# Optimization experiments

Measured on AMD Instinct MI355X. Metric: run time of the kernel, lower is better.

Reference implementation:

```python
import jax, jax.numpy as jnp
import numpy as np

B, NS, S, H = 512, 2, 128, 768
DS, NL = 384, 40
TEMP, ALPHA, GAMMA = 0.05, 0.15, 7.5
EPS = 1e-8


def setup_inputs() -> dict:
    key = jax.random.key(0)
    ks = jax.random.split(key, 8)
    return {
        "bert_emb": jax.random.normal(ks[0], (B, NS, S, H), dtype=jnp.float32),
        "rel_desc_emb": jax.random.normal(ks[1], (B, DS), dtype=jnp.float32),
        "dense_w": 0.02 * jax.random.normal(ks[2], (H, H), dtype=jnp.float32),
        "dense_b": jnp.zeros((H,), dtype=jnp.float32),
        "cls_w": 0.02 * jax.random.normal(ks[3], (3 * H, NL), dtype=jnp.float32),
        "cls_b": jnp.zeros((NL,), dtype=jnp.float32),
        "fc_w": 0.02 * jax.random.normal(ks[4], (3 * H, DS), dtype=jnp.float32),
        "fc_b": jnp.zeros((DS,), dtype=jnp.float32),
        "entity_idx": jax.random.randint(ks[5], (B, NS, 2), 0, S, dtype=jnp.int64 if jax.config.jax_enable_x64 else jnp.int32),
        "classify_labels": jax.random.randint(ks[6], (B,), 0, NL, dtype=jnp.int64 if jax.config.jax_enable_x64 else jnp.int32),
    }


def _mean_ce(logits, labels):
    lp = jax.nn.log_softmax(logits, axis=-1)
    return -jnp.mean(jnp.take_along_axis(lp, labels[:, None], axis=1))


def _l2n(x):
    return x / jnp.maximum(jnp.linalg.norm(x, axis=-1, keepdims=True), EPS)


def reference(bert_emb, rel_desc_emb, dense_w, dense_b, cls_w, cls_b, fc_w, fc_b,
              entity_idx, classify_labels):
    b = bert_emb.shape[0]
    bidx = jnp.arange(b)
    # ----- relation representation from sentence 0 (cls | head | tail) -----
    s0 = bert_emb[:, 0]                                   # [B,S,H]
    cls_tok = s0[:, 0]                                    # [B,H]
    head = s0[bidx, entity_idx[:, 0, 0]]                  # [B,H]
    tail = s0[bidx, entity_idx[:, 0, 1]]                  # [B,H]
    relation_hidden = jnp.tanh(jnp.concatenate([cls_tok, head, tail], axis=-1))  # [B,3H]
    logits = relation_hidden @ cls_w + cls_b              # [B,NL]
    ce_loss = _mean_ce(logits, classify_labels)
    # ----- margin loss vs relation-description embeddings (cosine) -----
    rel_emb = relation_hidden @ fc_w + fc_b               # [B,DS]
    C = _l2n(rel_emb) @ _l2n(rel_desc_emb).T              # [B,B] cosine sims
    pos = jnp.diagonal(C)
    diff_label = classify_labels[:, None] != classify_labels[None, :]
    neg = jnp.max(jnp.where(diff_label, C, -jnp.inf), axis=1)
    neg = jnp.maximum(neg, 0.0)                           # max_val initialized at 0
    margin_loss = jnp.sum(jax.nn.relu(neg - pos + GAMMA)) * (1.0 - ALPHA)
    ce_loss = ce_loss + margin_loss
    # ----- contrastive loss on (head|tail) entity pairs from both sents -----
    # dense is token-wise; apply only to the 4 gathered tokens per example
    h1a = bert_emb[bidx, 0, entity_idx[:, 0, 0]]
    h1b = bert_emb[bidx, 0, entity_idx[:, 0, 1]]
    h2a = bert_emb[bidx, 1, entity_idx[:, 1, 0]]
    h2b = bert_emb[bidx, 1, entity_idx[:, 1, 1]]
    toks = jnp.stack([h1a, h1b, h2a, h2b], axis=1)        # [B,4,H]
    toks = jnp.tanh(toks @ dense_w + dense_b)             # [B,4,H]
    z1 = toks[:, 0:2].reshape(b, -1)                      # [B,2H]
    z2 = toks[:, 2:4].reshape(b, -1)                      # [B,2H]
    cos_sim = (_l2n(z1) @ _l2n(z2).T) / TEMP              # [B,B]
    cl_loss = _mean_ce(cos_sim, bidx)
    return ce_loss + ALPHA * cl_loss
```

## Files before the change

### kernel.cpp

```cpp
#include <hip/hip_runtime.h>
#include <hip/hip_bf16.h>
#include <math.h>

#define B_   512
#define NS_  2
#define S_   128
#define H_   768
#define DS_  384
#define NL_  40
#define H3_  (3*H_)
#define TEMP_ 0.05f
#define ALPHA_ 0.15f
#define GAMMA_ 7.5f
#define EPS_ 1e-8f

typedef __attribute__((ext_vector_type(8))) short bf8_t;
typedef __attribute__((ext_vector_type(4))) float f4_t;

#define LDSPAD 40


__device__ __forceinline__ float block_reduce_sum(float v, float* sh) {
    int t = threadIdx.x;
    sh[t] = v; __syncthreads();
    for (int s = blockDim.x / 2; s > 0; s >>= 1) {
        if (t < s) sh[t] += sh[t + s];
        __syncthreads();
    }
    float r = sh[0]; __syncthreads();
    return r;
}

__device__ __forceinline__ float block_reduce_max(float v, float* sh) {
    int t = threadIdx.x;
    sh[t] = v; __syncthreads();
    for (int s = blockDim.x / 2; s > 0; s >>= 1) {
        if (t < s) sh[t] = fmaxf(sh[t], sh[t + s]);
        __syncthreads();
    }
    float r = sh[0]; __syncthreads();
    return r;
}

__device__ __forceinline__ void transpose_tile(
    const float* __restrict__ in, __hip_bfloat16* __restrict__ out,
    int K, int N, int kt, int nt, int tid, float* tileLds )
{
    int k0 = kt * 32, n0 = nt * 32;
    int tx = tid & 31, ty = tid >> 5;
#pragma unroll
    for (int i = 0; i < 4; ++i) {
        int k = k0 + ty + i * 8, n = n0 + tx;
        if (k < K && n < N) tileLds[(ty + i*8) * 33 + tx] = in[(size_t)k * N + n];
    }
    __syncthreads();
#pragma unroll
    for (int i = 0; i < 4; ++i) {
        int n = n0 + ty + i * 8, k = k0 + tx;
        if (n < N && k < K) out[(size_t)n * K + k] = __float2bfloat16(tileLds[tx * 33 + ty + i*8]);
    }
}

__global__ __launch_bounds__(256) void prep_kernel(
    const float* __restrict__ bert, const int* __restrict__ eidx,
    const float* __restrict__ dense_w, const float* __restrict__ fc_w,
    const float* __restrict__ cls_w, const float* __restrict__ desc,
    __hip_bfloat16* __restrict__ rh_bf, __hip_bfloat16* __restrict__ toks_bf,
    __hip_bfloat16* __restrict__ dwt, __hip_bfloat16* __restrict__ fwt,
    __hip_bfloat16* __restrict__ cwt, __hip_bfloat16* __restrict__ desc_nb,
    float* __restrict__ acc, int* __restrict__ done)
{
    __shared__ float tileLds[32 * 33];
    int blk = blockIdx.x;
    int t = threadIdx.x;
    if (blk < 512) {
        int b = blk;
        if (b == 0) {
            if (t < 4) acc[t] = 0.0f;
            if (t == 4) *done = 0;
        }
        int e00 = eidx[b*4 + 0];
        int e01 = eidx[b*4 + 1];
        int e10 = eidx[b*4 + 2];
        int e11 = eidx[b*4 + 3];
        const float* s0 = bert + (size_t)b * NS_ * S_ * H_;
        const float* s1 = s0 + (size_t)S_ * H_;
        const float* cls  = s0;
        const float* head = s0 + (size_t)e00 * H_;
        const float* tail = s0 + (size_t)e01 * H_;
        const float* h2a  = s1 + (size_t)e10 * H_;
        const float* h2b  = s1 + (size_t)e11 * H_;
        __hip_bfloat16* rhb = rh_bf + (size_t)b * H3_;
        __hip_bfloat16* tk  = toks_bf + (size_t)b * 4 * H_;
        for (int h = t; h < H_; h += 256) {
            float c  = cls[h];
            float hd = head[h];
            float tl = tail[h];
            rhb[h]        = __float2bfloat16(tanhf(c));
            rhb[H_ + h]   = __float2bfloat16(tanhf(hd));
            rhb[2*H_ + h] = __float2bfloat16(tanhf(tl));
            tk[h]         = __float2bfloat16(hd);
            tk[H_ + h]    = __float2bfloat16(tl);
            tk[2*H_ + h]  = __float2bfloat16(h2a[h]);
            tk[3*H_ + h]  = __float2bfloat16(h2b[h]);
        }
    } else if (blk < 1088) {
        int q = blk - 512;
        transpose_tile(dense_w, dwt, H_, H_, q / 24, q % 24, t, tileLds);
    } else if (blk < 1952) {
        int q = blk - 1088;
        transpose_tile(fc_w, fwt, H3_, DS_, q / 12, q % 12, t, tileLds);
    } else if (blk < 2096) {
        int q = blk - 1952;
        int kt = q / 2, nt = q % 2;
        transpose_tile(cls_w, cwt, H3_, NL_, kt, nt, t, tileLds);
        if (nt == 1) {
            int tx = t & 31, ty = t >> 5;
            cwt[(size_t)(40 + ty) * H3_ + kt * 32 + tx] = __float2bfloat16(0.0f);
        }
    } else {
        int i = blk - 2096;
        const float* x = desc + (size_t)i * DS_;
        float ss = 0.0f;
        for (int d = t; d < DS_; d += 256) { float v = x[d]; ss += v * v; }
        ss = block_reduce_sum(ss, tileLds);
        float inv = 1.0f / fmaxf(sqrtf(ss), EPS_);
        __hip_bfloat16* o = desc_nb + (size_t)i * DS_;
        for (int d = t; d < DS_; d += 256) o[d] = __float2bfloat16(x[d] * inv);
    }
}


__device__ __forceinline__ void gemm128_body(
    const __hip_bfloat16* __restrict__ A, const __hip_bfloat16* __restrict__ Bp,
    const float* __restrict__ bias, float* __restrict__ C,
    int K, int lda, int ldb, int ldc, int fuse_tanh, int bx, int by,
    __hip_bfloat16* As, __hip_bfloat16* Bs)
{
    int tid  = threadIdx.x;
    int lane = tid & 63;
    int wave = tid >> 6;
    int wm = (wave >> 1) * 64;
    int wn = (wave & 1) * 64;
    int lr = lane & 15;
    int quad = lane >> 4;
    int rowBase = by * 128;
    int colBase = bx * 128;

    f4_t acc[4][4];
#pragma unroll
    for (int i = 0; i < 4; ++i)
#pragma unroll
        for (int j = 0; j < 4; ++j) acc[i][j] = (f4_t){0.f, 0.f, 0.f, 0.f};

    int sr = tid >> 2, sc = tid & 3;
    for (int k0 = 0; k0 < K; k0 += 32) {
#pragma unroll
        for (int half = 0; half < 2; ++half) {
            int r = sr + half * 64;
            *(bf8_t*)&As[r * LDSPAD + sc * 8] =
                *(const bf8_t*)(A + (size_t)(rowBase + r) * lda + k0 + sc * 8);
            *(bf8_t*)&Bs[r * LDSPAD + sc * 8] =
                *(const bf8_t*)(Bp + (size_t)(colBase + r) * ldb + k0 + sc * 8);
        }
        __syncthreads();
        bf8_t af[4], bfr[4];
#pragma unroll
        for (int f = 0; f < 4; ++f) {
            af[f]  = *(const bf8_t*)&As[(wm + f*16 + lr) * LDSPAD + quad * 8];
            bfr[f] = *(const bf8_t*)&Bs[(wn + f*16 + lr) * LDSPAD + quad * 8];
        }
#pragma unroll
        for (int i = 0; i < 4; ++i)
#pragma unroll
            for (int j = 0; j < 4; ++j)
                acc[i][j] = __builtin_amdgcn_mfma_f32_16x16x32_bf16(af[i], bfr[j], acc[i][j], 0, 0, 0);
        __syncthreads();
    }
#pragma unroll
    for (int j = 0; j < 4; ++j) {
        int col = colBase + wn + j*16 + lr;
        float bv = bias ? bias[col] : 0.0f;
#pragma unroll
        for (int i = 0; i < 4; ++i) {
            int row0 = rowBase + wm + i*16 + quad*4;
#pragma unroll
            for (int r = 0; r < 4; ++r) {
                float v = acc[i][j][r] + bv;
                if (fuse_tanh) v = tanhf(v);
                C[(size_t)(row0 + r) * ldc + col] = v;
            }
        }
    }
}

__device__ __forceinline__ void gemm64_body(
    const __hip_bfloat16* __restrict__ A, const __hip_bfloat16* __restrict__ Bp,
    const float* __restrict__ bias, float* __restrict__ C,
    int K, int lda, int ldb, int ldc, float scale, int bx, int by,
    __hip_bfloat16* As, __hip_bfloat16* Bs)
{
    int tid  = threadIdx.x;
    int lane = tid & 63;
    int wave = tid >> 6;
    int lr = lane & 15;
    int quad = lane >> 4;
    int rowBase = by * 64;
    int colBase = bx * 64;

    f4_t acc[4];
#pragma unroll
    for (int i = 0; i < 4; ++i) acc[i] = (f4_t){0.f, 0.f, 0.f, 0.f};

    int sr = tid >> 2, sc = tid & 3;
    for (int k0 = 0; k0 < K; k0 += 32) {
        *(bf8_t*)&As[sr * LDSPAD + sc * 8] =
            *(const bf8_t*)(A + (size_t)(rowBase + sr) * lda + k0 + sc * 8);
        *(bf8_t*)&Bs[sr * LDSPAD + sc * 8] =
            *(const bf8_t*)(Bp + (size_t)(colBase + sr) * ldb + k0 + sc * 8);
        __syncthreads();
        bf8_t bfr = *(const bf8_t*)&Bs[(wave*16 + lr) * LDSPAD + quad * 8];
#pragma unroll
        for (int f = 0; f < 4; ++f) {
            bf8_t af = *(const bf8_t*)&As[(f*16 + lr) * LDSPAD + quad * 8];
            acc[f] = __builtin_amdgcn_mfma_f32_16x16x32_bf16(af, bfr, acc[f], 0, 0, 0);
        }
        __syncthreads();
    }
    int col = colBase + wave*16 + lr;
    float bv = bias ? bias[col] : 0.0f;
#pragma unroll
    for (int f = 0; f < 4; ++f) {
        int row0 = rowBase + f*16 + quad*4;
#pragma unroll
        for (int r = 0; r < 4; ++r)
            C[(size_t)(row0 + r) * ldc + col] = acc[f][r] * scale + bv;
    }
}

__device__ __forceinline__ void cls_ce_body(
    const __hip_bfloat16* __restrict__ rh, const __hip_bfloat16* __restrict__ cwt,
    const float* __restrict__ cls_b, const int* __restrict__ labels,
    float* __restrict__ acc, int rowBase, float* lgp )
{
    int tid  = threadIdx.x;
    int lane = tid & 63;
    int wave = tid >> 6;
    int lr = lane & 15;
    int quad = lane >> 4;

    f4_t a3[3];
#pragma unroll
    for (int j = 0; j < 3; ++j) a3[j] = (f4_t){0.f, 0.f, 0.f, 0.f};

    int kw0 = wave * (H3_ / 4);
    const __hip_bfloat16* aRow = rh + (size_t)(rowBase + lr) * H3_ + quad * 8;
#pragma unroll 2
    for (int s = 0; s < 18; ++s) {
        int k = kw0 + s * 32;
        bf8_t af = *(const bf8_t*)(aRow + k);
#pragma unroll
        for (int j = 0; j < 3; ++j) {
            bf8_t bfr = *(const bf8_t*)(cwt + (size_t)(j*16 + lr) * H3_ + k + quad * 8);
            a3[j] = __builtin_amdgcn_mfma_f32_16x16x32_bf16(af, bfr, a3[j], 0, 0, 0);
        }
    }
#pragma unroll
    for (int j = 0; j < 3; ++j) {
        int col = j*16 + lr;
#pragma unroll
        for (int r = 0; r < 4; ++r)
            lgp[wave * 768 + (quad*4 + r) * 48 + col] = a3[j][r];
    }
    __syncthreads();
    for (int idx = tid; idx < 768; idx += 256) {
        int col = idx % 48;
        float s = lgp[idx] + lgp[768 + idx] + lgp[1536 + idx] + lgp[2304 + idx];
        s = (col < NL_) ? (s + cls_b[col]) : -INFINITY;
        lgp[idx] = s;
    }
    __syncthreads();
    if (tid < 64) {
        float ce = 0.0f;
        if (tid < 16) {
            const float* Lr = &lgp[tid * 48];
            float m = -INFINITY;
            for (int c = 0; c < NL_; ++c) m = fmaxf(m, Lr[c]);
            float s = 0.0f;
            for (int c = 0; c < NL_; ++c) s += expf(Lr[c] - m);
            ce = logf(s) + m - Lr[labels[rowBase + tid]];
        }
        for (int off = 8; off >= 1; off >>= 1) ce += __shfl_down(ce, off);
        if (tid == 0) atomicAdd(acc + 0, ce * (1.0f / (float)B_));
    }
}

__global__ __launch_bounds__(256) void gemms_kernel(
    const __hip_bfloat16* __restrict__ toks_bf, const __hip_bfloat16* __restrict__ dwt,
    const float* __restrict__ dense_b, float* __restrict__ toks_out,
    const __hip_bfloat16* __restrict__ rh_bf, const __hip_bfloat16* __restrict__ fwt,
    const float* __restrict__ fc_b, float* __restrict__ rel_emb,
    const __hip_bfloat16* __restrict__ cwt, const float* __restrict__ cls_b,
    const int* __restrict__ labels, float* __restrict__ acc)
{
    __shared__ __align__(16) char smem[2 * 128 * LDSPAD * 2];
    int blk = blockIdx.x;
    if (blk < 96) {
        gemm128_body(toks_bf, dwt, dense_b, toks_out, H_, H_, H_, H_, 1,
                     blk % 6, blk / 6,
                     (__hip_bfloat16*)smem, (__hip_bfloat16*)(smem + 128 * LDSPAD * 2));
    } else if (blk < 144) {
        int q = blk - 96;
        gemm64_body(rh_bf, fwt, fc_b, rel_emb, H3_, H3_, H3_, DS_, 1.0f,
                    q % 6, q / 6,
                    (__hip_bfloat16*)smem, (__hip_bfloat16*)(smem + 64 * LDSPAD * 2));
    } else {
        cls_ce_body(rh_bf, cwt, cls_b, labels, acc, (blk - 144) * 16, (float*)smem);
    }
}

__global__ __launch_bounds__(256) void znorm_kernel(
    const float* __restrict__ rel_emb, const float* __restrict__ toks_out,
    __hip_bfloat16* __restrict__ rel_nb, __hip_bfloat16* __restrict__ z_bf)
{
    __shared__ float sh[256];
    int blk = blockIdx.x, t = threadIdx.x;
    const float* x; __hip_bfloat16* o; int D;
    if (blk < 512) { x = rel_emb + (size_t)blk * DS_;          o = rel_nb + (size_t)blk * DS_;        D = DS_; }
    else           { x = toks_out + (size_t)(blk-512) * 2*H_;  o = z_bf + (size_t)(blk-512) * 2*H_;   D = 2*H_; }
    float ss = 0.0f;
    for (int d = t; d < D; d += 256) { float v = x[d]; ss += v * v; }
    ss = block_reduce_sum(ss, sh);
    float inv = 1.0f / fmaxf(sqrtf(ss), EPS_);
    for (int d = t; d < D; d += 256) o[d] = __float2bfloat16(x[d] * inv);
}

__global__ __launch_bounds__(256) void c1c2_kernel(
    const __hip_bfloat16* __restrict__ rel_nb, const __hip_bfloat16* __restrict__ desc_nb,
    const __hip_bfloat16* __restrict__ z_bf, float* __restrict__ C1, float* __restrict__ C2)
{
    __shared__ __align__(16) char smem[2 * 64 * LDSPAD * 2];
    __hip_bfloat16* As = (__hip_bfloat16*)smem;
    __hip_bfloat16* Bs = (__hip_bfloat16*)(smem + 64 * LDSPAD * 2);
    int blk = blockIdx.x;
    if (blk < 64) {
        gemm64_body(rel_nb, desc_nb, (const float*)nullptr, C1, DS_, DS_, DS_, B_, 1.0f,
                    blk % 8, blk / 8, As, Bs);
    } else {
        int q = blk - 64;
        gemm64_body(z_bf, z_bf + 2*H_, (const float*)nullptr, C2, 2*H_, 4*H_, 4*H_, B_, 1.0f/TEMP_,
                    q % 8, q / 8, As, Bs);
    }
}

__global__ __launch_bounds__(256) void tail_kernel(
    const float* __restrict__ C1, const float* __restrict__ C2,
    const int* __restrict__ labels, float* __restrict__ acc,
    int* __restrict__ done, float* __restrict__ out)
{
    __shared__ float sh[256];
    int blk = blockIdx.x, t = threadIdx.x;
    if (blk < 512) {
        int i = blk;
        int li = labels[i];
        const float* row = C1 + (size_t)i * B_;
        float m = -INFINITY;
        for (int j = t; j < B_; j += 256)
            if (labels[j] != li) m = fmaxf(m, row[j]);
        float negmax = block_reduce_max(m, sh);
        if (t == 0) {
            float neg = fmaxf(negmax, 0.0f);
            float term = neg - row[i] + GAMMA_;
            if (term > 0.0f) atomicAdd(acc + 1, term);
        }
    } else {
        int i = blk - 512;
        const float* row = C2 + (size_t)i * B_;
        float m = -INFINITY;
        for (int j = t; j < B_; j += 256) m = fmaxf(m, row[j]);
        m = block_reduce_max(m, sh);
        float s = 0.0f;
        for (int j = t; j < B_; j += 256) s += expf(row[j] - m);
        s = block_reduce_sum(s, sh);
        if (t == 0) atomicAdd(acc + 2, (logf(s) + m - row[i]) * (1.0f / (float)B_));
    }
    __threadfence();
    if (t == 0) {
        int prev = atomicAdd(done, 1);
        if (prev == 1023) {
            float a0 = atomicAdd(acc + 0, 0.0f);
            float a1 = atomicAdd(acc + 1, 0.0f);
            float a2 = atomicAdd(acc + 2, 0.0f);
            out[0] = a0 + (1.0f - ALPHA_) * a1 + ALPHA_ * a2;
        }
    }
}


extern "C" void kernel_launch(void* const* d_in, const int* in_sizes, int n_in,
                              void* d_out, int out_size, void* d_ws, size_t ws_size,
                              hipStream_t stream) {
    const float* bert     = (const float*)d_in[0];
    const float* desc     = (const float*)d_in[1];
    const float* dense_w  = (const float*)d_in[2];
    const float* dense_b  = (const float*)d_in[3];
    const float* cls_w    = (const float*)d_in[4];
    const float* cls_b    = (const float*)d_in[5];
    const float* fc_w     = (const float*)d_in[6];
    const float* fc_b     = (const float*)d_in[7];
    const int*   eidx     = (const int*)d_in[8];
    const int*   labels   = (const int*)d_in[9];
    float* out = (float*)d_out;

    float* fp = (float*)d_ws;
    __hip_bfloat16* rh_bf   = (__hip_bfloat16*)fp; fp += (size_t)B_*H3_/2;
    __hip_bfloat16* toks_bf = (__hip_bfloat16*)fp; fp += (size_t)B_*4*H_/2;
    __hip_bfloat16* dwt_bf  = (__hip_bfloat16*)fp; fp += (size_t)H_*H_/2;
    __hip_bfloat16* fwt_bf  = (__hip_bfloat16*)fp; fp += (size_t)DS_*H3_/2;
    __hip_bfloat16* cwt_bf  = (__hip_bfloat16*)fp; fp += (size_t)48*H3_/2;
    __hip_bfloat16* desc_nb = (__hip_bfloat16*)fp; fp += (size_t)B_*DS_/2;
    __hip_bfloat16* rel_nb  = (__hip_bfloat16*)fp; fp += (size_t)B_*DS_/2;
    __hip_bfloat16* z_bf    = (__hip_bfloat16*)fp; fp += (size_t)B_*4*H_/2;
    float* toks_out = fp; fp += (size_t)B_*4*H_;
    float* rel_emb  = fp; fp += (size_t)B_*DS_;
    float* C1       = fp; fp += (size_t)B_*B_;
    float* C2       = fp; fp += (size_t)B_*B_;
    float* acc      = fp; fp += 4;
    int*   done     = (int*)fp;

    prep_kernel<<<2608, 256, 0, stream>>>(bert, eidx, dense_w, fc_w, cls_w, desc,
                                          rh_bf, toks_bf, dwt_bf, fwt_bf, cwt_bf,
                                          desc_nb, acc, done);

    gemms_kernel<<<176, 256, 0, stream>>>(toks_bf, dwt_bf, dense_b, toks_out,
                                          rh_bf, fwt_bf, fc_b, rel_emb,
                                          cwt_bf, cls_b, labels, acc);

    znorm_kernel<<<1536, 256, 0, stream>>>(rel_emb, toks_out, rel_nb, z_bf);

    c1c2_kernel<<<128, 256, 0, stream>>>(rel_nb, desc_nb, z_bf, C1, C2);

    tail_kernel<<<1024, 256, 0, stream>>>(C1, C2, labels, acc, done, out);
}
```

Baseline: 571.7 us.

## Double-buffer GEMM LDS tiles, split-K small GEMMs, shuffle-based reductions

Both GEMM bodies now use double-buffered LDS and prefetch the next K tile into registers while MFMAs run, so there is one barrier per iteration instead of two. The fc GEMM and the z GEMM are split along K into two halves written to separate partial buffers, which gives the grid more blocks. The halves are summed, with the bias added, in znorm and tail. Block reductions switch to wave shuffles plus a 4-entry LDS combine, and znorm and tail use vectorized loads with fixed per-thread element counts. This costs extra workspace and extra partial-buffer traffic, and it doubles LDS per block.

```diff
diff --git a/kernel.cpp b/kernel.cpp
--- a/kernel.cpp
+++ b/kernel.cpp
@@ -15,30 +15,36 @@
 #define EPS_ 1e-8f
 
 typedef __attribute__((ext_vector_type(8))) short bf8_t;
+typedef __attribute__((ext_vector_type(4))) short s4_t;
 typedef __attribute__((ext_vector_type(4))) float f4_t;
 
 #define LDSPAD 40
 
 
+__device__ __forceinline__ short bfbits(float x) {
+    __hip_bfloat16 h = __float2bfloat16(x);
+    return *reinterpret_cast<short*>(&h);
+}
+
 __device__ __forceinline__ float block_reduce_sum(float v, float* sh) {
-    int t = threadIdx.x;
-    sh[t] = v; __syncthreads();
-    for (int s = blockDim.x / 2; s > 0; s >>= 1) {
-        if (t < s) sh[t] += sh[t + s];
-        __syncthreads();
-    }
-    float r = sh[0]; __syncthreads();
+#pragma unroll
+    for (int off = 32; off >= 1; off >>= 1) v += __shfl_down(v, off, 64);
+    int w = threadIdx.x >> 6;
+    if ((threadIdx.x & 63) == 0) sh[w] = v;
+    __syncthreads();
+    float r = (sh[0] + sh[1]) + (sh[2] + sh[3]);
+    __syncthreads();
     return r;
 }
 
 __device__ __forceinline__ float block_reduce_max(float v, float* sh) {
-    int t = threadIdx.x;
-    sh[t] = v; __syncthreads();
-    for (int s = blockDim.x / 2; s > 0; s >>= 1) {
-        if (t < s) sh[t] = fmaxf(sh[t], sh[t + s]);
-        __syncthreads();
-    }
-    float r = sh[0]; __syncthreads();
+#pragma unroll
+    for (int off = 32; off >= 1; off >>= 1) v = fmaxf(v, __shfl_down(v, off, 64));
+    int w = threadIdx.x >> 6;
+    if ((threadIdx.x & 63) == 0) sh[w] = v;
+    __syncthreads();
+    float r = fmaxf(fmaxf(sh[0], sh[1]), fmaxf(sh[2], sh[3]));
+    __syncthreads();
     return r;
 }
 
@@ -135,7 +141,8 @@
     const __hip_bfloat16* __restrict__ A, const __hip_bfloat16* __restrict__ Bp,
     const float* __restrict__ bias, float* __restrict__ C,
     int K, int lda, int ldb, int ldc, int fuse_tanh, int bx, int by,
-    __hip_bfloat16* As, __hip_bfloat16* Bs)
+    __hip_bfloat16* As0, __hip_bfloat16* Bs0,
+    __hip_bfloat16* As1, __hip_bfloat16* Bs1)
 {
     int tid  = threadIdx.x;
     int lane = tid & 63;
@@ -154,27 +161,48 @@
         for (int j = 0; j < 4; ++j) acc[i][j] = (f4_t){0.f, 0.f, 0.f, 0.f};
 
     int sr = tid >> 2, sc = tid & 3;
-    for (int k0 = 0; k0 < K; k0 += 32) {
-#pragma unroll
-        for (int half = 0; half < 2; ++half) {
-            int r = sr + half * 64;
-            *(bf8_t*)&As[r * LDSPAD + sc * 8] =
-                *(const bf8_t*)(A + (size_t)(rowBase + r) * lda + k0 + sc * 8);
-            *(bf8_t*)&Bs[r * LDSPAD + sc * 8] =
-                *(const bf8_t*)(Bp + (size_t)(colBase + r) * ldb + k0 + sc * 8);
-        }
-        __syncthreads();
+    const __hip_bfloat16* Abase = A + (size_t)(rowBase + sr) * lda + sc * 8;
+    const __hip_bfloat16* Bbase = Bp + (size_t)(colBase + sr) * ldb + sc * 8;
+    size_t a64 = (size_t)64 * lda, b64 = (size_t)64 * ldb;
+
+    *(bf8_t*)&As0[sr * LDSPAD + sc * 8]        = *(const bf8_t*)(Abase);
+    *(bf8_t*)&As0[(sr + 64) * LDSPAD + sc * 8] = *(const bf8_t*)(Abase + a64);
+    *(bf8_t*)&Bs0[sr * LDSPAD + sc * 8]        = *(const bf8_t*)(Bbase);
+    *(bf8_t*)&Bs0[(sr + 64) * LDSPAD + sc * 8] = *(const bf8_t*)(Bbase + b64);
+    __syncthreads();
+
+    int nIter = K >> 5;
+    for (int i = 0; i < nIter; ++i) {
+        __hip_bfloat16* Asc = (i & 1) ? As1 : As0;
+        __hip_bfloat16* Bsc = (i & 1) ? Bs1 : Bs0;
+        __hip_bfloat16* Asn = (i & 1) ? As0 : As1;
+        __hip_bfloat16* Bsn = (i & 1) ? Bs0 : Bs1;
+        bf8_t pa0, pa1, pb0, pb1;
+        bool pf = (i + 1 < nIter);
+        if (pf) {
+            int k = (i + 1) << 5;
+            pa0 = *(const bf8_t*)(Abase + k);
+            pa1 = *(const bf8_t*)(Abase + a64 + k);
+            pb0 = *(const bf8_t*)(Bbase + k);
+            pb1 = *(const bf8_t*)(Bbase + b64 + k);
+        }
         bf8_t af[4], bfr[4];
 #pragma unroll
         for (int f = 0; f < 4; ++f) {
-            af[f]  = *(const bf8_t*)&As[(wm + f*16 + lr) * LDSPAD + quad * 8];
-            bfr[f] = *(const bf8_t*)&Bs[(wn + f*16 + lr) * LDSPAD + quad * 8];
-        }
-#pragma unroll
-        for (int i = 0; i < 4; ++i)
+            af[f]  = *(const bf8_t*)&Asc[(wm + f*16 + lr) * LDSPAD + quad * 8];
+            bfr[f] = *(const bf8_t*)&Bsc[(wn + f*16 + lr) * LDSPAD + quad * 8];
+        }
+#pragma unroll
+        for (int ii = 0; ii < 4; ++ii)
 #pragma unroll
             for (int j = 0; j < 4; ++j)
-                acc[i][j] = __builtin_amdgcn_mfma_f32_16x16x32_bf16(af[i], bfr[j], acc[i][j], 0, 0, 0);
+                acc[ii][j] = __builtin_amdgcn_mfma_f32_16x16x32_bf16(af[ii], bfr[j], acc[ii][j], 0, 0, 0);
+        if (pf) {
+            *(bf8_t*)&Asn[sr * LDSPAD + sc * 8]        = pa0;
+            *(bf8_t*)&Asn[(sr + 64) * LDSPAD + sc * 8] = pa1;
+            *(bf8_t*)&Bsn[sr * LDSPAD + sc * 8]        = pb0;
+            *(bf8_t*)&Bsn[(sr + 64) * LDSPAD + sc * 8] = pb1;
+        }
         __syncthreads();
     }
 #pragma unroll
@@ -196,9 +224,10 @@
 
 __device__ __forceinline__ void gemm64_body(
     const __hip_bfloat16* __restrict__ A, const __hip_bfloat16* __restrict__ Bp,
-    const float* __restrict__ bias, float* __restrict__ C,
-    int K, int lda, int ldb, int ldc, float scale, int bx, int by,
-    __hip_bfloat16* As, __hip_bfloat16* Bs)
+    float* __restrict__ C,
+    int K, int kBase, int lda, int ldb, int ldc, float scale, int bx, int by,
+    __hip_bfloat16* As0, __hip_bfloat16* Bs0,
+    __hip_bfloat16* As1, __hip_bfloat16* Bs1)
 {
     int tid  = threadIdx.x;
     int lane = tid & 63;
@@ -213,28 +242,45 @@
     for (int i = 0; i < 4; ++i) acc[i] = (f4_t){0.f, 0.f, 0.f, 0.f};
 
     int sr = tid >> 2, sc = tid & 3;
-    for (int k0 = 0; k0 < K; k0 += 32) {
-        *(bf8_t*)&As[sr * LDSPAD + sc * 8] =
-            *(const bf8_t*)(A + (size_t)(rowBase + sr) * lda + k0 + sc * 8);
-        *(bf8_t*)&Bs[sr * LDSPAD + sc * 8] =
-            *(const bf8_t*)(Bp + (size_t)(colBase + sr) * ldb + k0 + sc * 8);
+    const __hip_bfloat16* Abase = A + (size_t)(rowBase + sr) * lda + kBase + sc * 8;
+    const __hip_bfloat16* Bbase = Bp + (size_t)(colBase + sr) * ldb + kBase + sc * 8;
+
+    *(bf8_t*)&As0[sr * LDSPAD + sc * 8] = *(const bf8_t*)(Abase);
+    *(bf8_t*)&Bs0[sr * LDSPAD + sc * 8] = *(const bf8_t*)(Bbase);
+    __syncthreads();
+
+    int nIter = K >> 5;
+    for (int i = 0; i < nIter; ++i) {
+        __hip_bfloat16* Asc = (i & 1) ? As1 : As0;
+        __hip_bfloat16* Bsc = (i & 1) ? Bs1 : Bs0;
+        __hip_bfloat16* Asn = (i & 1) ? As0 : As1;
+        __hip_bfloat16* Bsn = (i & 1) ? Bs0 : Bs1;
+        bf8_t pa, pb;
+        bool pf = (i + 1 < nIter);
+        if (pf) {
+            int k = (i + 1) << 5;
+            pa = *(const bf8_t*)(Abase + k);
+            pb = *(const bf8_t*)(Bbase + k);
+        }
+        bf8_t bfr = *(const bf8_t*)&Bsc[(wave*16 + lr) * LDSPAD + quad * 8];
+#pragma unroll
+        for (int f = 0; f < 4; ++f) {
+            bf8_t af = *(const bf8_t*)&Asc[(f*16 + lr) * LDSPAD + quad * 8];
+            acc[f] = __builtin_amdgcn_mfma_f32_16x16x32_bf16(af, bfr, acc[f], 0, 0, 0);
+        }
+        if (pf) {
+            *(bf8_t*)&Asn[sr * LDSPAD + sc * 8] = pa;
+            *(bf8_t*)&Bsn[sr * LDSPAD + sc * 8] = pb;
+        }
         __syncthreads();
-        bf8_t bfr = *(const bf8_t*)&Bs[(wave*16 + lr) * LDSPAD + quad * 8];
-#pragma unroll
-        for (int f = 0; f < 4; ++f) {
-            bf8_t af = *(const bf8_t*)&As[(f*16 + lr) * LDSPAD + quad * 8];
-            acc[f] = __builtin_amdgcn_mfma_f32_16x16x32_bf16(af, bfr, acc[f], 0, 0, 0);
-        }
-        __syncthreads();
     }
     int col = colBase + wave*16 + lr;
-    float bv = bias ? bias[col] : 0.0f;
 #pragma unroll
     for (int f = 0; f < 4; ++f) {
         int row0 = rowBase + f*16 + quad*4;
 #pragma unroll
         for (int r = 0; r < 4; ++r)
-            C[(size_t)(row0 + r) * ldc + col] = acc[f][r] * scale + bv;
+            C[(size_t)(row0 + r) * ldc + col] = acc[f][r] * scale;
     }
 }
 
@@ -299,74 +345,110 @@
     const __hip_bfloat16* __restrict__ toks_bf, const __hip_bfloat16* __restrict__ dwt,
     const float* __restrict__ dense_b, float* __restrict__ toks_out,
     const __hip_bfloat16* __restrict__ rh_bf, const __hip_bfloat16* __restrict__ fwt,
-    const float* __restrict__ fc_b, float* __restrict__ rel_emb,
+    float* __restrict__ relP0, float* __restrict__ relP1,
     const __hip_bfloat16* __restrict__ cwt, const float* __restrict__ cls_b,
     const int* __restrict__ labels, float* __restrict__ acc)
 {
-    __shared__ __align__(16) char smem[2 * 128 * LDSPAD * 2];
+    __shared__ __align__(16) char smem[4 * 128 * LDSPAD * 2];
+    __hip_bfloat16* s0 = (__hip_bfloat16*)smem;
     int blk = blockIdx.x;
     if (blk < 96) {
         gemm128_body(toks_bf, dwt, dense_b, toks_out, H_, H_, H_, H_, 1,
                      blk % 6, blk / 6,
-                     (__hip_bfloat16*)smem, (__hip_bfloat16*)(smem + 128 * LDSPAD * 2));
-    } else if (blk < 144) {
+                     s0, s0 + 128*LDSPAD, s0 + 2*128*LDSPAD, s0 + 3*128*LDSPAD);
+    } else if (blk < 192) {
         int q = blk - 96;
-        gemm64_body(rh_bf, fwt, fc_b, rel_emb, H3_, H3_, H3_, DS_, 1.0f,
-                    q % 6, q / 6,
-                    (__hip_bfloat16*)smem, (__hip_bfloat16*)(smem + 64 * LDSPAD * 2));
+        int half = q >= 48 ? 1 : 0;
+        int q2 = q - 48 * half;
+        gemm64_body(rh_bf, fwt, half ? relP1 : relP0, H3_/2, half * (H3_/2),
+                    H3_, H3_, DS_, 1.0f, q2 % 6, q2 / 6,
+                    s0, s0 + 64*LDSPAD, s0 + 2*64*LDSPAD, s0 + 3*64*LDSPAD);
     } else {
-        cls_ce_body(rh_bf, cwt, cls_b, labels, acc, (blk - 144) * 16, (float*)smem);
+        cls_ce_body(rh_bf, cwt, cls_b, labels, acc, (blk - 192) * 16, (float*)smem);
     }
 }
 
 __global__ __launch_bounds__(256) void znorm_kernel(
-    const float* __restrict__ rel_emb, const float* __restrict__ toks_out,
+    const float* __restrict__ relP0, const float* __restrict__ relP1,
+    const float* __restrict__ fc_b, const float* __restrict__ toks_out,
     __hip_bfloat16* __restrict__ rel_nb, __hip_bfloat16* __restrict__ z_bf)
 {
-    __shared__ float sh[256];
+    __shared__ float sh[4];
     int blk = blockIdx.x, t = threadIdx.x;
-    const float* x; __hip_bfloat16* o; int D;
-    if (blk < 512) { x = rel_emb + (size_t)blk * DS_;          o = rel_nb + (size_t)blk * DS_;        D = DS_; }
-    else           { x = toks_out + (size_t)(blk-512) * 2*H_;  o = z_bf + (size_t)(blk-512) * 2*H_;   D = 2*H_; }
-    float ss = 0.0f;
-    for (int d = t; d < D; d += 256) { float v = x[d]; ss += v * v; }
-    ss = block_reduce_sum(ss, sh);
-    float inv = 1.0f / fmaxf(sqrtf(ss), EPS_);
-    for (int d = t; d < D; d += 256) o[d] = __float2bfloat16(x[d] * inv);
+    if (blk < 512) {
+        const f4_t* p0 = (const f4_t*)(relP0 + (size_t)blk * DS_);
+        const f4_t* p1 = (const f4_t*)(relP1 + (size_t)blk * DS_);
+        const f4_t* bb = (const f4_t*)fc_b;
+        f4_t v = (f4_t){0.f, 0.f, 0.f, 0.f};
+        float ss = 0.0f;
+        if (t < 96) {
+            v = p0[t] + p1[t] + bb[t];
+            ss = v[0]*v[0] + v[1]*v[1] + v[2]*v[2] + v[3]*v[3];
+        }
+        ss = block_reduce_sum(ss, sh);
+        float inv = 1.0f / fmaxf(sqrtf(ss), EPS_);
+        if (t < 96) {
+            s4_t o = { bfbits(v[0]*inv), bfbits(v[1]*inv), bfbits(v[2]*inv), bfbits(v[3]*inv) };
+            ((s4_t*)(rel_nb + (size_t)blk * DS_))[t] = o;
+        }
+    } else {
+        int r = blk - 512;
+        const f4_t* xv = (const f4_t*)(toks_out + (size_t)r * 2 * H_);
+        f4_t v0 = xv[t];
+        f4_t v1 = (t < 128) ? xv[256 + t] : (f4_t){0.f, 0.f, 0.f, 0.f};
+        float ss = v0[0]*v0[0] + v0[1]*v0[1] + v0[2]*v0[2] + v0[3]*v0[3]
+                 + v1[0]*v1[0] + v1[1]*v1[1] + v1[2]*v1[2] + v1[3]*v1[3];
+        ss = block_reduce_sum(ss, sh);
+        float inv = 1.0f / fmaxf(sqrtf(ss), EPS_);
+        s4_t* ov = (s4_t*)(z_bf + (size_t)r * 2 * H_);
+        s4_t o0 = { bfbits(v0[0]*inv), bfbits(v0[1]*inv), bfbits(v0[2]*inv), bfbits(v0[3]*inv) };
+        ov[t] = o0;
+        if (t < 128) {
+            s4_t o1 = { bfbits(v1[0]*inv), bfbits(v1[1]*inv), bfbits(v1[2]*inv), bfbits(v1[3]*inv) };
+            ov[256 + t] = o1;
+        }
+    }
 }
 
 __global__ __launch_bounds__(256) void c1c2_kernel(
     const __hip_bfloat16* __restrict__ rel_nb, const __hip_bfloat16* __restrict__ desc_nb,
-    const __hip_bfloat16* __restrict__ z_bf, float* __restrict__ C1, float* __restrict__ C2)
-{
-    __shared__ __align__(16) char smem[2 * 64 * LDSPAD * 2];
-    __hip_bfloat16* As = (__hip_bfloat16*)smem;
-    __hip_bfloat16* Bs = (__hip_bfloat16*)(smem + 64 * LDSPAD * 2);
+    const __hip_bfloat16* __restrict__ z_bf,
+    float* __restrict__ C1, float* __restrict__ C2a, float* __restrict__ C2b)
+{
+    __shared__ __align__(16) char smem[4 * 64 * LDSPAD * 2];
+    __hip_bfloat16* s0 = (__hip_bfloat16*)smem;
+    __hip_bfloat16* As0 = s0;
+    __hip_bfloat16* Bs0 = s0 + 64*LDSPAD;
+    __hip_bfloat16* As1 = s0 + 2*64*LDSPAD;
+    __hip_bfloat16* Bs1 = s0 + 3*64*LDSPAD;
     int blk = blockIdx.x;
     if (blk < 64) {
-        gemm64_body(rel_nb, desc_nb, (const float*)nullptr, C1, DS_, DS_, DS_, B_, 1.0f,
-                    blk % 8, blk / 8, As, Bs);
+        gemm64_body(rel_nb, desc_nb, C1, DS_, 0, DS_, DS_, B_, 1.0f,
+                    blk % 8, blk / 8, As0, Bs0, As1, Bs1);
     } else {
         int q = blk - 64;
-        gemm64_body(z_bf, z_bf + 2*H_, (const float*)nullptr, C2, 2*H_, 4*H_, 4*H_, B_, 1.0f/TEMP_,
-                    q % 8, q / 8, As, Bs);
+        int half = q >= 64 ? 1 : 0;
+        int q2 = q - 64 * half;
+        gemm64_body(z_bf, z_bf + 2*H_, half ? C2b : C2a, H_, half * H_,
+                    4*H_, 4*H_, B_, 1.0f/TEMP_, q2 % 8, q2 / 8, As0, Bs0, As1, Bs1);
     }
 }
 
 __global__ __launch_bounds__(256) void tail_kernel(
-    const float* __restrict__ C1, const float* __restrict__ C2,
+    const float* __restrict__ C1, const float* __restrict__ C2a, const float* __restrict__ C2b,
     const int* __restrict__ labels, float* __restrict__ acc,
     int* __restrict__ done, float* __restrict__ out)
 {
-    __shared__ float sh[256];
+    __shared__ float sh[4];
     int blk = blockIdx.x, t = threadIdx.x;
     if (blk < 512) {
         int i = blk;
         int li = labels[i];
         const float* row = C1 + (size_t)i * B_;
+        int j0 = t, j1 = t + 256;
         float m = -INFINITY;
-        for (int j = t; j < B_; j += 256)
-            if (labels[j] != li) m = fmaxf(m, row[j]);
+        if (labels[j0] != li) m = row[j0];
+        if (labels[j1] != li) m = fmaxf(m, row[j1]);
         float negmax = block_reduce_max(m, sh);
         if (t == 0) {
             float neg = fmaxf(negmax, 0.0f);
@@ -375,14 +457,18 @@
         }
     } else {
         int i = blk - 512;
-        const float* row = C2 + (size_t)i * B_;
-        float m = -INFINITY;
-        for (int j = t; j < B_; j += 256) m = fmaxf(m, row[j]);
-        m = block_reduce_max(m, sh);
-        float s = 0.0f;
-        for (int j = t; j < B_; j += 256) s += expf(row[j] - m);
+        const float* ra = C2a + (size_t)i * B_;
+        const float* rb = C2b + (size_t)i * B_;
+        int j0 = t, j1 = t + 256;
+        float va = ra[j0] + rb[j0];
+        float vb = ra[j1] + rb[j1];
+        float m = block_reduce_max(fmaxf(va, vb), sh);
+        float s = expf(va - m) + expf(vb - m);
         s = block_reduce_sum(s, sh);
-        if (t == 0) atomicAdd(acc + 2, (logf(s) + m - row[i]) * (1.0f / (float)B_));
+        if (t == 0) {
+            float pos = ra[i] + rb[i];
+            atomicAdd(acc + 2, (logf(s) + m - pos) * (1.0f / (float)B_));
+        }
     }
     __threadfence();
     if (t == 0) {
@@ -422,9 +508,11 @@
     __hip_bfloat16* rel_nb  = (__hip_bfloat16*)fp; fp += (size_t)B_*DS_/2;
     __hip_bfloat16* z_bf    = (__hip_bfloat16*)fp; fp += (size_t)B_*4*H_/2;
     float* toks_out = fp; fp += (size_t)B_*4*H_;
-    float* rel_emb  = fp; fp += (size_t)B_*DS_;
+    float* relP0    = fp; fp += (size_t)B_*DS_;
+    float* relP1    = fp; fp += (size_t)B_*DS_;
     float* C1       = fp; fp += (size_t)B_*B_;
-    float* C2       = fp; fp += (size_t)B_*B_;
+    float* C2a      = fp; fp += (size_t)B_*B_;
+    float* C2b      = fp; fp += (size_t)B_*B_;
     float* acc      = fp; fp += 4;
     int*   done     = (int*)fp;
 
@@ -432,13 +520,13 @@
                                           rh_bf, toks_bf, dwt_bf, fwt_bf, cwt_bf,
                                           desc_nb, acc, done);
 
-    gemms_kernel<<<176, 256, 0, stream>>>(toks_bf, dwt_bf, dense_b, toks_out,
-                                          rh_bf, fwt_bf, fc_b, rel_emb,
+    gemms_kernel<<<224, 256, 0, stream>>>(toks_bf, dwt_bf, dense_b, toks_out,
+                                          rh_bf, fwt_bf, relP0, relP1,
                                           cwt_bf, cls_b, labels, acc);
 
-    znorm_kernel<<<1536, 256, 0, stream>>>(rel_emb, toks_out, rel_nb, z_bf);
-
-    c1c2_kernel<<<128, 256, 0, stream>>>(rel_nb, desc_nb, z_bf, C1, C2);
-
-    tail_kernel<<<1024, 256, 0, stream>>>(C1, C2, labels, acc, done, out);
-}
+    znorm_kernel<<<1536, 256, 0, stream>>>(relP0, relP1, fc_b, toks_out, rel_nb, z_bf);
+
+    c1c2_kernel<<<192, 256, 0, stream>>>(rel_nb, desc_nb, z_bf, C1, C2a, C2b);
+
+    tail_kernel<<<1024, 256, 0, stream>>>(C1, C2a, C2b, labels, acc, done, out);
+}
```

After: 549.7 us. -3.9%, faster.
